# Optimization experiments

Measured on AMD Instinct MI355X. Metric: run time of the kernel, lower is better.

The kernel has to match this reference:

```python
import jax, jax.numpy as jnp
import numpy as np

GLYPH_DIM = 4096
PADDING_IDX = GLYPH_DIM  # 4096
GLYPH_EMB = 20           # CHAR_EMB 16 + COLOR_EMB 4
HIDDEN = 32
MAX_LEN = 64


def setup_inputs() -> dict:
    key = jax.random.key(0)
    k1, k2, k3, k4, k5, k6, k7 = jax.random.split(key, 7)
    B, H, W = 8192, 21, 79
    glyph_chars = jax.random.randint(k1, (B, H, W), 0, 256, dtype=jnp.int32)
    glyph_colors = jax.random.randint(k2, (B, H, W), 0, 16, dtype=jnp.int32)
    # Embedding table with zero padding row (torch padding_idx semantics)
    emb_table = jax.random.normal(k3, (GLYPH_DIM + 1, GLYPH_EMB), dtype=jnp.float32) * 0.02
    emb_table = emb_table.at[PADDING_IDX].set(0.0)
    s = 1.0 / np.sqrt(HIDDEN)
    W_ih = jax.random.uniform(k4, (HIDDEN, GLYPH_EMB), minval=-s, maxval=s, dtype=jnp.float32)
    W_hh = jax.random.uniform(k5, (HIDDEN, HIDDEN), minval=-s, maxval=s, dtype=jnp.float32)
    b_ih = jax.random.uniform(k6, (HIDDEN,), minval=-s, maxval=s, dtype=jnp.float32)
    b_hh = jax.random.uniform(k7, (HIDDEN,), minval=-s, maxval=s, dtype=jnp.float32)
    return {"glyph_chars": glyph_chars, "glyph_colors": glyph_colors,
            "emb_table": emb_table, "W_ih": W_ih, "W_hh": W_hh,
            "b_ih": b_ih, "b_hh": b_hh}


def _encode_bag(glyph_chars, glyph_colors):
    """Batched sorted-unique compaction over the bounded glyph id range."""
    B = glyph_chars.shape[0]
    g_ids = ((glyph_chars << 4) + glyph_colors).reshape(B, -1)  # [B, H*W]
    # presence[b, g] = glyph g appears in sample b (batched histogram)
    bidx = jnp.broadcast_to(jnp.arange(B, dtype=g_ids.dtype)[:, None], g_ids.shape)
    presence = jnp.zeros((B, GLYPH_DIM), dtype=bool).at[bidx, g_ids].set(True)
    # compact: present ids keep their value, absent become PADDING_IDX (=4096),
    # so sorting yields ascending unique ids followed by padding.
    ids = jnp.arange(GLYPH_DIM, dtype=jnp.int32)
    keys = jnp.where(presence, ids, jnp.int32(PADDING_IDX))
    bag = jnp.sort(keys, axis=1)[:, :MAX_LEN]  # [B, MAX_LEN]
    lengths = jnp.minimum(presence.sum(axis=1), MAX_LEN)  # [B]
    return bag, lengths


def reference(glyph_chars, glyph_colors, emb_table, W_ih, W_hh, b_ih, b_hh):
    bag, lengths = _encode_bag(glyph_chars, glyph_colors)
    emb = emb_table[bag]  # [B, MAX_LEN, GLYPH_EMB]
    B = emb.shape[0]

    # packed RNN == plain RNN where hidden state freezes past each sequence length
    xs = jnp.swapaxes(emb, 0, 1)  # [T, B, E]

    def step(h, inp):
        xt, t = inp
        h_new = jnp.tanh(xt @ W_ih.T + b_ih + h @ W_hh.T + b_hh)
        h = jnp.where((t < lengths)[:, None], h_new, h)
        return h, None

    h0 = jnp.zeros((B, HIDDEN), dtype=emb.dtype)
    h, _ = jax.lax.scan(step, h0, (xs, jnp.arange(MAX_LEN)))
    return (h, emb, bag)
```

## Files before the change

kernel.cpp:

```cpp
#include <hip/hip_runtime.h>

#define HW 1659
#define PADID 4096
#define EMB 20
#define HID 32
#define MAXLEN 64

__global__ __launch_bounds__(256) void bag_emb_kernel(
    const int* __restrict__ chars, const int* __restrict__ colors,
    const float* __restrict__ emb_table,
    float* __restrict__ out_emb, float* __restrict__ out_bag)
{
    __shared__ unsigned char pres[4096];
    __shared__ int bagl[64];
    __shared__ int wsum[4];

    const int b   = blockIdx.x;
    const int tid = threadIdx.x;
    const int lane = tid & 63;
    const int wv   = tid >> 6;

    ((uint4*)pres)[tid] = make_uint4(0u, 0u, 0u, 0u);
    if (tid < 64) bagl[tid] = PADID;
    __syncthreads();

    const int base = b * HW;
    const int pe = (4 - (base & 3)) & 3;
    if (tid < pe) {
        int g = (chars[base + tid] << 4) + colors[base + tid];
        pres[g] = 1;
    }
    const int nv = (HW - pe) >> 2;
    const int nt = HW - pe - (nv << 2);
    const int4* c4 = (const int4*)(chars + base + pe);
    const int4* k4 = (const int4*)(colors + base + pe);
    for (int v = tid; v < nv; v += 256) {
        int4 c = c4[v], k = k4[v];
        pres[(c.x << 4) + k.x] = 1;
        pres[(c.y << 4) + k.y] = 1;
        pres[(c.z << 4) + k.z] = 1;
        pres[(c.w << 4) + k.w] = 1;
    }
    if (tid < nt) {
        int i = base + pe + (nv << 2) + tid;
        int g = (chars[i] << 4) + colors[i];
        pres[g] = 1;
    }
    __syncthreads();

    uint4 w4 = ((const uint4*)pres)[tid];
    const unsigned M = 0x01010101u;
    int cnt = __popc(w4.x & M) + __popc(w4.y & M)
            + __popc(w4.z & M) + __popc(w4.w & M);

    int pre = cnt;
#pragma unroll
    for (int d = 1; d < 64; d <<= 1) {
        int v = __shfl_up(pre, d, 64);
        if (lane >= d) pre += v;
    }
    if (lane == 63) wsum[wv] = pre;
    __syncthreads();
    int wbase = 0;
#pragma unroll
    for (int w2 = 0; w2 < 4; w2++) wbase += (w2 < wv) ? wsum[w2] : 0;
    int p = wbase + pre - cnt;

    unsigned wrd[4] = {w4.x, w4.y, w4.z, w4.w};
#pragma unroll
    for (int c = 0; c < 4; c++) {
#pragma unroll
        for (int k = 0; k < 4; k++) {
            if ((wrd[c] >> (8 * k)) & 1) {
                if (p < 64) bagl[p] = 16 * tid + 4 * c + k;
                p++;
            }
        }
    }
    __syncthreads();

    if (tid < 64) out_bag[(size_t)b * 64 + tid] = (float)bagl[tid];

    const float4* tab4 = (const float4*)emb_table;
    float4* dst4 = (float4*)(out_emb + (size_t)b * (MAXLEN * EMB));
    for (int q = tid; q < MAXLEN * 5; q += 256) {
        int t = q / 5;
        int m = q - t * 5;
        int row = bagl[t];
        dst4[q] = tab4[row * 5 + m];
    }
}

__global__ __launch_bounds__(128, 4) void rnn_kernel(
    const float* __restrict__ emb, const float* __restrict__ bagf,
    const float* __restrict__ W_ih, const float* __restrict__ W_hh,
    const float* __restrict__ b_ih, const float* __restrict__ b_hh,
    float* __restrict__ out_h)
{
    __shared__ float hbuf[4][32];

    const int tid = threadIdx.x;
    const int ib  = tid >> 5;
    const int j   = tid & 31;
    const int b   = blockIdx.x * 4 + ib;

    float wih[EMB];
#pragma unroll
    for (int k = 0; k < EMB; k++) wih[k] = W_ih[j * EMB + k];
    float whh[HID];
#pragma unroll
    for (int k = 0; k < HID; k++) whh[k] = W_hh[j * HID + k];
#pragma unroll
    for (int k = 0; k < EMB; k++) asm("" : "+v"(wih[k]));
#pragma unroll
    for (int k = 0; k < HID; k++) asm("" : "+v"(whh[k]));
    const float sbias = b_ih[j] + b_hh[j];

    const float* bp = bagf + (size_t)b * 64;
    unsigned long long m0 = __ballot(bp[j]      < 4095.5f);
    unsigned long long m1 = __ballot(bp[32 + j] < 4095.5f);
    const int half = ib & 1;
    const int len = __popc((unsigned)(m0 >> (half * 32)))
                  + __popc((unsigned)(m1 >> (half * 32)));

    hbuf[ib][j] = 0.f;
    asm volatile("s_waitcnt lgkmcnt(0)" ::: "memory");

    float h = 0.f;
    const float* xb = emb + (size_t)b * (MAXLEN * EMB);

    for (int t = 0; t < MAXLEN; t++) {
        const float4* xp = (const float4*)(xb + t * EMB);
        float4 x0 = xp[0], x1 = xp[1], x2 = xp[2], x3 = xp[3], x4 = xp[4];

        float s = sbias;
        const float4* hb4 = (const float4*)hbuf[ib];
#pragma unroll
        for (int m = 0; m < 8; m++) {
            float4 hv = hb4[m];
            s += whh[4*m+0]*hv.x + whh[4*m+1]*hv.y
               + whh[4*m+2]*hv.z + whh[4*m+3]*hv.w;
        }
        s += wih[0]*x0.x + wih[1]*x0.y + wih[2]*x0.z + wih[3]*x0.w;
        s += wih[4]*x1.x + wih[5]*x1.y + wih[6]*x1.z + wih[7]*x1.w;
        s += wih[8]*x2.x + wih[9]*x2.y + wih[10]*x2.z + wih[11]*x2.w;
        s += wih[12]*x3.x + wih[13]*x3.y + wih[14]*x3.z + wih[15]*x3.w;
        s += wih[16]*x4.x + wih[17]*x4.y + wih[18]*x4.z + wih[19]*x4.w;

        s = fminf(fmaxf(s, -9.f), 9.f);
        float e = __expf(2.f * s);
        float th = (e - 1.f) * __builtin_amdgcn_rcpf(e + 1.f);

        h = (t < len) ? th : h;

        hbuf[ib][j] = h;
        asm volatile("s_waitcnt lgkmcnt(0)" ::: "memory");
    }

    out_h[(size_t)b * HID + j] = h;
}

extern "C" void kernel_launch(void* const* d_in, const int* in_sizes, int n_in,
                              void* d_out, int out_size, void* d_ws, size_t ws_size,
                              hipStream_t stream) {
    const int*   chars     = (const int*)d_in[0];
    const int*   colors    = (const int*)d_in[1];
    const float* emb_table = (const float*)d_in[2];
    const float* W_ih      = (const float*)d_in[3];
    const float* W_hh      = (const float*)d_in[4];
    const float* b_ih      = (const float*)d_in[5];
    const float* b_hh      = (const float*)d_in[6];

    const int B = in_sizes[0] / HW;

    float* out     = (float*)d_out;
    float* out_h   = out;
    float* out_emb = out + (size_t)B * HID;
    float* out_bag = out_emb + (size_t)B * MAXLEN * EMB;

    bag_emb_kernel<<<B, 256, 0, stream>>>(chars, colors, emb_table, out_emb, out_bag);
    rnn_kernel<<<B / 4, 128, 0, stream>>>(out_emb, out_bag, W_ih, W_hh, b_ih, b_hh, out_h);
}
```

Baseline: 198.8 us.

## Fuse bag compaction, embedding gather and RNN into one kernel

Merges the bag/embedding kernel and the RNN kernel into a single kernel where each 128-thread block handles four samples. The presence bitmap shares LDS with an embedding buffer that the RNN then reads directly, instead of re-reading the emb and bag outputs from global memory. This removes a second launch and the global round trip, at the cost of fewer threads per sample during the histogram phase and serialised phases inside each block that may reduce overlap.

```diff
diff --git a/kernel.cpp b/kernel.cpp
--- a/kernel.cpp
+++ b/kernel.cpp
@@ -5,104 +5,113 @@
 #define EMB 20
 #define HID 32
 #define MAXLEN 64
+#define SPB 4
 
-__global__ __launch_bounds__(256) void bag_emb_kernel(
+__global__ __launch_bounds__(128, 4) void fused_kernel(
     const int* __restrict__ chars, const int* __restrict__ colors,
     const float* __restrict__ emb_table,
-    float* __restrict__ out_emb, float* __restrict__ out_bag)
+    const float* __restrict__ W_ih, const float* __restrict__ W_hh,
+    const float* __restrict__ b_ih, const float* __restrict__ b_hh,
+    float* __restrict__ out_h, float* __restrict__ out_emb,
+    float* __restrict__ out_bag)
 {
-    __shared__ unsigned char pres[4096];
-    __shared__ int bagl[64];
-    __shared__ int wsum[4];
+    __shared__ __align__(16) unsigned char smem_raw[SPB * MAXLEN * EMB * 4];
+    unsigned char (*pres)[4096]      = (unsigned char (*)[4096])smem_raw;
+    float (*xbuf)[MAXLEN][EMB]       = (float (*)[MAXLEN][EMB])smem_raw;
+    __shared__ int bagl[SPB][64];
+    __shared__ float hbuf[SPB][HID];
 
-    const int b   = blockIdx.x;
-    const int tid = threadIdx.x;
-    const int lane = tid & 63;
-    const int wv   = tid >> 6;
+    const int tid   = threadIdx.x;
+    const int lane  = tid & 63;
+    const int wv    = tid >> 6;
+    const int gbase = blockIdx.x * SPB;
 
-    ((uint4*)pres)[tid] = make_uint4(0u, 0u, 0u, 0u);
-    if (tid < 64) bagl[tid] = PADID;
-    __syncthreads();
-
-    const int base = b * HW;
-    const int pe = (4 - (base & 3)) & 3;
-    if (tid < pe) {
-        int g = (chars[base + tid] << 4) + colors[base + tid];
-        pres[g] = 1;
-    }
-    const int nv = (HW - pe) >> 2;
-    const int nt = HW - pe - (nv << 2);
-    const int4* c4 = (const int4*)(chars + base + pe);
-    const int4* k4 = (const int4*)(colors + base + pe);
-    for (int v = tid; v < nv; v += 256) {
-        int4 c = c4[v], k = k4[v];
-        pres[(c.x << 4) + k.x] = 1;
-        pres[(c.y << 4) + k.y] = 1;
-        pres[(c.z << 4) + k.z] = 1;
-        pres[(c.w << 4) + k.w] = 1;
-    }
-    if (tid < nt) {
-        int i = base + pe + (nv << 2) + tid;
-        int g = (chars[i] << 4) + colors[i];
-        pres[g] = 1;
+    ((int*)bagl)[tid]       = PADID;
+    ((int*)bagl)[tid + 128] = PADID;
+    {
+        uint4* p4 = (uint4*)smem_raw;
+#pragma unroll
+        for (int i = 0; i < 8; i++) p4[tid + 128 * i] = make_uint4(0u, 0u, 0u, 0u);
     }
     __syncthreads();
 
-    uint4 w4 = ((const uint4*)pres)[tid];
-    const unsigned M = 0x01010101u;
-    int cnt = __popc(w4.x & M) + __popc(w4.y & M)
-            + __popc(w4.z & M) + __popc(w4.w & M);
+    for (int s = 0; s < SPB; s++) {
+        const int base = (gbase + s) * HW;
+        unsigned char* pr = pres[s];
+        const int pe = (4 - (base & 3)) & 3;
+        if (tid < pe) {
+            int g = (chars[base + tid] << 4) + colors[base + tid];
+            pr[g] = 1;
+        }
+        const int nv = (HW - pe) >> 2;
+        const int nt = HW - pe - (nv << 2);
+        const int4* c4 = (const int4*)(chars + base + pe);
+        const int4* k4 = (const int4*)(colors + base + pe);
+        for (int v = tid; v < nv; v += 128) {
+            int4 c = c4[v], k = k4[v];
+            pr[(c.x << 4) + k.x] = 1;
+            pr[(c.y << 4) + k.y] = 1;
+            pr[(c.z << 4) + k.z] = 1;
+            pr[(c.w << 4) + k.w] = 1;
+        }
+        if (tid < nt) {
+            int i = base + pe + (nv << 2) + tid;
+            pr[(chars[i] << 4) + colors[i]] = 1;
+        }
+    }
+    __syncthreads();
 
-    int pre = cnt;
+    for (int si = 0; si < 2; si++) {
+        const int s = 2 * wv + si;
+        const uint4* p4 = (const uint4*)pres[s];
+        uint4 a = p4[4 * lane + 0], b2 = p4[4 * lane + 1];
+        uint4 c = p4[4 * lane + 2], d  = p4[4 * lane + 3];
+        const unsigned M = 0x01010101u;
+        int cnt = __popc(a.x & M) + __popc(a.y & M) + __popc(a.z & M) + __popc(a.w & M)
+                + __popc(b2.x & M) + __popc(b2.y & M) + __popc(b2.z & M) + __popc(b2.w & M)
+                + __popc(c.x & M) + __popc(c.y & M) + __popc(c.z & M) + __popc(c.w & M)
+                + __popc(d.x & M) + __popc(d.y & M) + __popc(d.z & M) + __popc(d.w & M);
+        int pre = cnt;
 #pragma unroll
-    for (int d = 1; d < 64; d <<= 1) {
-        int v = __shfl_up(pre, d, 64);
-        if (lane >= d) pre += v;
-    }
-    if (lane == 63) wsum[wv] = pre;
-    __syncthreads();
-    int wbase = 0;
+        for (int dd = 1; dd < 64; dd <<= 1) {
+            int v = __shfl_up(pre, dd, 64);
+            if (lane >= dd) pre += v;
+        }
+        int p = pre - cnt;
+        unsigned wrd[16] = {a.x, a.y, a.z, a.w, b2.x, b2.y, b2.z, b2.w,
+                            c.x, c.y, c.z, c.w, d.x, d.y, d.z, d.w};
 #pragma unroll
-    for (int w2 = 0; w2 < 4; w2++) wbase += (w2 < wv) ? wsum[w2] : 0;
-    int p = wbase + pre - cnt;
-
-    unsigned wrd[4] = {w4.x, w4.y, w4.z, w4.w};
+        for (int wi = 0; wi < 16; wi++) {
 #pragma unroll
-    for (int c = 0; c < 4; c++) {
-#pragma unroll
-        for (int k = 0; k < 4; k++) {
-            if ((wrd[c] >> (8 * k)) & 1) {
-                if (p < 64) bagl[p] = 16 * tid + 4 * c + k;
-                p++;
+            for (int k = 0; k < 4; k++) {
+                if ((wrd[wi] >> (8 * k)) & 1) {
+                    if (p < 64) bagl[s][p] = 64 * lane + 4 * wi + k;
+                    p++;
+                }
             }
         }
     }
     __syncthreads();
 
-    if (tid < 64) out_bag[(size_t)b * 64 + tid] = (float)bagl[tid];
+    out_bag[(size_t)gbase * 64 + tid]       = (float)((int*)bagl)[tid];
+    out_bag[(size_t)gbase * 64 + 128 + tid] = (float)((int*)bagl)[tid + 128];
 
     const float4* tab4 = (const float4*)emb_table;
-    float4* dst4 = (float4*)(out_emb + (size_t)b * (MAXLEN * EMB));
-    for (int q = tid; q < MAXLEN * 5; q += 256) {
-        int t = q / 5;
-        int m = q - t * 5;
-        int row = bagl[t];
-        dst4[q] = tab4[row * 5 + m];
+    float4* dstb = (float4*)(out_emb + (size_t)gbase * (MAXLEN * EMB));
+    for (int q = tid; q < SPB * MAXLEN * 5; q += 128) {
+        int s = q / 320;
+        int r = q - 320 * s;
+        int t = r / 5;
+        int m = r - 5 * t;
+        int row = bagl[s][t];
+        float4 val = tab4[row * 5 + m];
+        dstb[q] = val;
+        ((float4*)&xbuf[s][t][0])[m] = val;
     }
-}
+    __syncthreads();
 
-__global__ __launch_bounds__(128, 4) void rnn_kernel(
-    const float* __restrict__ emb, const float* __restrict__ bagf,
-    const float* __restrict__ W_ih, const float* __restrict__ W_hh,
-    const float* __restrict__ b_ih, const float* __restrict__ b_hh,
-    float* __restrict__ out_h)
-{
-    __shared__ float hbuf[4][32];
-
-    const int tid = threadIdx.x;
-    const int ib  = tid >> 5;
-    const int j   = tid & 31;
-    const int b   = blockIdx.x * 4 + ib;
+    const int ib = tid >> 5;
+    const int j  = tid & 31;
 
     float wih[EMB];
 #pragma unroll
@@ -111,14 +120,13 @@
 #pragma unroll
     for (int k = 0; k < HID; k++) whh[k] = W_hh[j * HID + k];
 #pragma unroll
-    for (int k = 0; k < EMB; k++) asm("" : "+v"(wih[k]));
+    for (int k = 0; k < EMB; k++) asm volatile("" : "+v"(wih[k]));
 #pragma unroll
-    for (int k = 0; k < HID; k++) asm("" : "+v"(whh[k]));
+    for (int k = 0; k < HID; k++) asm volatile("" : "+v"(whh[k]));
     const float sbias = b_ih[j] + b_hh[j];
 
-    const float* bp = bagf + (size_t)b * 64;
-    unsigned long long m0 = __ballot(bp[j]      < 4095.5f);
-    unsigned long long m1 = __ballot(bp[32 + j] < 4095.5f);
+    unsigned long long m0 = __ballot(bagl[ib][j]      < PADID);
+    unsigned long long m1 = __ballot(bagl[ib][32 + j] < PADID);
     const int half = ib & 1;
     const int len = __popc((unsigned)(m0 >> (half * 32)))
                   + __popc((unsigned)(m1 >> (half * 32)));
@@ -127,10 +135,8 @@
     asm volatile("s_waitcnt lgkmcnt(0)" ::: "memory");
 
     float h = 0.f;
-    const float* xb = emb + (size_t)b * (MAXLEN * EMB);
-
     for (int t = 0; t < MAXLEN; t++) {
-        const float4* xp = (const float4*)(xb + t * EMB);
+        const float4* xp = (const float4*)&xbuf[ib][t][0];
         float4 x0 = xp[0], x1 = xp[1], x2 = xp[2], x3 = xp[3], x4 = xp[4];
 
         float s = sbias;
@@ -157,7 +163,7 @@
         asm volatile("s_waitcnt lgkmcnt(0)" ::: "memory");
     }
 
-    out_h[(size_t)b * HID + j] = h;
+    out_h[(size_t)(gbase + ib) * HID + j] = h;
 }
 
 extern "C" void kernel_launch(void* const* d_in, const int* in_sizes, int n_in,
@@ -178,6 +184,7 @@
     float* out_emb = out + (size_t)B * HID;
     float* out_bag = out_emb + (size_t)B * MAXLEN * EMB;
 
-    bag_emb_kernel<<<B, 256, 0, stream>>>(chars, colors, emb_table, out_emb, out_bag);
-    rnn_kernel<<<B / 4, 128, 0, stream>>>(out_emb, out_bag, W_ih, W_hh, b_ih, b_hh, out_h);
+    fused_kernel<<<B / SPB, 128, 0, stream>>>(chars, colors, emb_table,
+                                              W_ih, W_hh, b_ih, b_hh,
+                                              out_h, out_emb, out_bag);
 }
```

Result: slower. 209.5 us (+5.4%).

## Precompute embedding-times-W_ih projection table and gather it in RNN

Applied to the files above, without the earlier changes.

Adds a small kernel that multiplies every embedding table row by W_ih, giving a 4097x32 projection table in workspace. The RNN kernel then does one gathered load per step instead of reading 20 embedding floats and doing 20 FMAs per step. It also drops the per-thread wih registers and the asm register pins on whh. This needs enough workspace; otherwise it falls back to the old kernel. It adds an extra launch, plus dependent gather loads that hit a cache-resident table.

```diff
diff --git a/kernel.cpp b/kernel.cpp
--- a/kernel.cpp
+++ b/kernel.cpp
@@ -5,6 +5,22 @@
 #define EMB 20
 #define HID 32
 #define MAXLEN 64
+
+__global__ __launch_bounds__(128) void proj_kernel(
+    const float* __restrict__ emb_table, const float* __restrict__ W_ih,
+    float* __restrict__ proj)
+{
+    const int tid = threadIdx.x;
+    const int g = blockIdx.x * 4 + (tid >> 5);
+    const int j = tid & 31;
+    if (g > PADID) return;
+    const float* er = emb_table + (size_t)g * EMB;
+    const float* wr = W_ih + j * EMB;
+    float s = 0.f;
+#pragma unroll
+    for (int k = 0; k < EMB; k++) s += wr[k] * er[k];
+    proj[(size_t)g * HID + j] = s;
+}
 
 __global__ __launch_bounds__(256) void bag_emb_kernel(
     const int* __restrict__ chars, const int* __restrict__ colors,
@@ -43,8 +59,7 @@
     }
     if (tid < nt) {
         int i = base + pe + (nv << 2) + tid;
-        int g = (chars[i] << 4) + colors[i];
-        pres[g] = 1;
+        pres[(chars[i] << 4) + colors[i]] = 1;
     }
     __syncthreads();
 
@@ -92,8 +107,8 @@
 }
 
 __global__ __launch_bounds__(128, 4) void rnn_kernel(
-    const float* __restrict__ emb, const float* __restrict__ bagf,
-    const float* __restrict__ W_ih, const float* __restrict__ W_hh,
+    const float* __restrict__ proj, const float* __restrict__ bagf,
+    const float* __restrict__ W_hh,
     const float* __restrict__ b_ih, const float* __restrict__ b_hh,
     float* __restrict__ out_h)
 {
@@ -104,16 +119,9 @@
     const int j   = tid & 31;
     const int b   = blockIdx.x * 4 + ib;
 
-    float wih[EMB];
-#pragma unroll
-    for (int k = 0; k < EMB; k++) wih[k] = W_ih[j * EMB + k];
     float whh[HID];
 #pragma unroll
     for (int k = 0; k < HID; k++) whh[k] = W_hh[j * HID + k];
-#pragma unroll
-    for (int k = 0; k < EMB; k++) asm("" : "+v"(wih[k]));
-#pragma unroll
-    for (int k = 0; k < HID; k++) asm("" : "+v"(whh[k]));
     const float sbias = b_ih[j] + b_hh[j];
 
     const float* bp = bagf + (size_t)b * 64;
@@ -127,12 +135,67 @@
     asm volatile("s_waitcnt lgkmcnt(0)" ::: "memory");
 
     float h = 0.f;
+    for (int t = 0; t < MAXLEN; t++) {
+        const int idx = (int)bp[t];
+        const float pv = proj[(size_t)idx * HID + j];
+
+        float s = sbias + pv;
+        const float4* hb4 = (const float4*)hbuf[ib];
+#pragma unroll
+        for (int m = 0; m < 8; m++) {
+            float4 hv = hb4[m];
+            s += whh[4*m+0]*hv.x + whh[4*m+1]*hv.y
+               + whh[4*m+2]*hv.z + whh[4*m+3]*hv.w;
+        }
+
+        s = fminf(fmaxf(s, -9.f), 9.f);
+        float e = __expf(2.f * s);
+        float th = (e - 1.f) * __builtin_amdgcn_rcpf(e + 1.f);
+
+        h = (t < len) ? th : h;
+
+        hbuf[ib][j] = h;
+        asm volatile("s_waitcnt lgkmcnt(0)" ::: "memory");
+    }
+
+    out_h[(size_t)b * HID + j] = h;
+}
+
+__global__ __launch_bounds__(128, 4) void rnn_kernel_noproj(
+    const float* __restrict__ emb, const float* __restrict__ bagf,
+    const float* __restrict__ W_ih, const float* __restrict__ W_hh,
+    const float* __restrict__ b_ih, const float* __restrict__ b_hh,
+    float* __restrict__ out_h)
+{
+    __shared__ float hbuf[4][32];
+    const int tid = threadIdx.x;
+    const int ib  = tid >> 5;
+    const int j   = tid & 31;
+    const int b   = blockIdx.x * 4 + ib;
+
+    float wih[EMB];
+#pragma unroll
+    for (int k = 0; k < EMB; k++) wih[k] = W_ih[j * EMB + k];
+    float whh[HID];
+#pragma unroll
+    for (int k = 0; k < HID; k++) whh[k] = W_hh[j * HID + k];
+    const float sbias = b_ih[j] + b_hh[j];
+
+    const float* bp = bagf + (size_t)b * 64;
+    unsigned long long m0 = __ballot(bp[j]      < 4095.5f);
+    unsigned long long m1 = __ballot(bp[32 + j] < 4095.5f);
+    const int half = ib & 1;
+    const int len = __popc((unsigned)(m0 >> (half * 32)))
+                  + __popc((unsigned)(m1 >> (half * 32)));
+
+    hbuf[ib][j] = 0.f;
+    asm volatile("s_waitcnt lgkmcnt(0)" ::: "memory");
+
+    float h = 0.f;
     const float* xb = emb + (size_t)b * (MAXLEN * EMB);
-
     for (int t = 0; t < MAXLEN; t++) {
         const float4* xp = (const float4*)(xb + t * EMB);
         float4 x0 = xp[0], x1 = xp[1], x2 = xp[2], x3 = xp[3], x4 = xp[4];
-
         float s = sbias;
         const float4* hb4 = (const float4*)hbuf[ib];
 #pragma unroll
@@ -146,17 +209,13 @@
         s += wih[8]*x2.x + wih[9]*x2.y + wih[10]*x2.z + wih[11]*x2.w;
         s += wih[12]*x3.x + wih[13]*x3.y + wih[14]*x3.z + wih[15]*x3.w;
         s += wih[16]*x4.x + wih[17]*x4.y + wih[18]*x4.z + wih[19]*x4.w;
-
         s = fminf(fmaxf(s, -9.f), 9.f);
         float e = __expf(2.f * s);
         float th = (e - 1.f) * __builtin_amdgcn_rcpf(e + 1.f);
-
         h = (t < len) ? th : h;
-
         hbuf[ib][j] = h;
         asm volatile("s_waitcnt lgkmcnt(0)" ::: "memory");
     }
-
     out_h[(size_t)b * HID + j] = h;
 }
 
@@ -178,6 +237,16 @@
     float* out_emb = out + (size_t)B * HID;
     float* out_bag = out_emb + (size_t)B * MAXLEN * EMB;
 
+    const size_t proj_bytes = (size_t)(PADID + 1) * HID * sizeof(float);
+
     bag_emb_kernel<<<B, 256, 0, stream>>>(chars, colors, emb_table, out_emb, out_bag);
-    rnn_kernel<<<B / 4, 128, 0, stream>>>(out_emb, out_bag, W_ih, W_hh, b_ih, b_hh, out_h);
-}
+
+    if (ws_size >= proj_bytes) {
+        float* proj = (float*)d_ws;
+        proj_kernel<<<(PADID + 1 + 3) / 4, 128, 0, stream>>>(emb_table, W_ih, proj);
+        rnn_kernel<<<B / 4, 128, 0, stream>>>(proj, out_bag, W_hh, b_ih, b_hh, out_h);
+    } else {
+        rnn_kernel_noproj<<<B / 4, 128, 0, stream>>>(out_emb, out_bag, W_ih, W_hh,
+                                                     b_ih, b_hh, out_h);
+    }
+}
```

Result: no change. 196.1 us (-1.3%).
